# Performance work log

Measured on AMD Instinct MI355X. Metric: run time of the kernel, lower is better.

## Reference

```python
import jax, jax.numpy as jnp
import numpy as np

B, T, C, H = 2, 2048, 1024, 16
D = C // H  # head_dim = 64

def setup_inputs() -> dict:
    key = jax.random.key(0)
    k0, k1, k2, k3, k4 = jax.random.split(key, 5)
    s = 1.0 / np.sqrt(C)
    return {
        "x": jax.random.normal(k0, (B, T, C), dtype=jnp.float32),
        "w_qkv": jax.random.uniform(k1, (C, 3 * C), jnp.float32, -s, s),
        "b_qkv": jax.random.uniform(k2, (3 * C,), jnp.float32, -s, s),
        "w_proj": jax.random.uniform(k3, (C, C), jnp.float32, -s, s),
        "b_proj": jax.random.uniform(k4, (C,), jnp.float32, -s, s),
    }

def reference(x, w_qkv, b_qkv, w_proj, b_proj):
    Bx, Tx, Cx = x.shape
    qkv = x @ w_qkv + b_qkv                      # [B,T,3C]
    q, k, v = jnp.split(qkv, 3, axis=-1)
    # [B,T,C] -> [B,H,T,D]
    def heads(t):
        return t.reshape(Bx, Tx, H, D).transpose(0, 2, 1, 3)
    q, k, v = heads(q), heads(k), heads(v)
    att = jnp.einsum('bhqd,bhkd->bhqk', q, k) / np.sqrt(D).astype(np.float32)
    causal = jnp.tril(jnp.ones((Tx, Tx), dtype=bool))
    att = jnp.where(causal, att, -jnp.inf)
    att = jax.nn.softmax(att, axis=-1)
    y = jnp.einsum('bhqk,bhkd->bhqd', att, v)    # [B,H,T,D]
    y = y.transpose(0, 2, 1, 3).reshape(Bx, Tx, Cx)
    return y @ w_proj + b_proj
```

## Files before the change

kernel.cpp:

```cpp
#include <hip/hip_runtime.h>

typedef short bf16x8 __attribute__((ext_vector_type(8)));
typedef float f32x4 __attribute__((ext_vector_type(4)));
typedef unsigned short u16;
typedef unsigned short u16x8 __attribute__((ext_vector_type(8)));
typedef unsigned short u16x4 __attribute__((ext_vector_type(4), may_alias));

__device__ __forceinline__ u16 f2bf(float f) {
    union { float f; unsigned u; } v; v.f = f;
    unsigned r = v.u + 0x7fffu + ((v.u >> 16) & 1u);
    return (u16)(r >> 16);
}
__device__ __forceinline__ u16 f2bf_rhu(float f) {
    union { float f; unsigned u; } v; v.f = f;
    return (u16)((v.u + 0x8000u) >> 16);
}

__device__ __forceinline__ void gld_lds16(const void* g, void* l) {
    __builtin_amdgcn_global_load_lds(
        (const __attribute__((address_space(1))) void*)g,
        (__attribute__((address_space(3))) void*)l, 16, 0, 0);
}

__global__ __launch_bounds__(256) void x_to_bf16(const float* __restrict__ in,
                                                 u16* __restrict__ out) {
    const int i = blockIdx.x * 256 + threadIdx.x;
    float4 a = ((const float4*)in)[i * 2];
    float4 b = ((const float4*)in)[i * 2 + 1];
    u16x8 h;
    h[0] = f2bf(a.x); h[1] = f2bf(a.y); h[2] = f2bf(a.z); h[3] = f2bf(a.w);
    h[4] = f2bf(b.x); h[5] = f2bf(b.y); h[6] = f2bf(b.z); h[7] = f2bf(b.w);
    *(u16x8*)(out + (size_t)i * 8) = h;
}

__global__ __launch_bounds__(256) void transpose_w(const float* __restrict__ in,
                                                   u16* __restrict__ out,
                                                   int K, int N) {
    __shared__ float tile[32][33];
    const int n0 = blockIdx.x * 32, k0 = blockIdx.y * 32;
    const int tx = threadIdx.x, ty = threadIdx.y;
#pragma unroll
    for (int i = 0; i < 32; i += 8)
        tile[ty + i][tx] = in[(size_t)(k0 + ty + i) * N + n0 + tx];
    __syncthreads();
#pragma unroll
    for (int i = 0; i < 32; i += 8)
        out[(size_t)(n0 + ty + i) * K + k0 + tx] = f2bf(tile[tx][ty + i]);
}

#define QSCALE 0.180336880f

template <int OUTMODE, int BN>
__global__ __launch_bounds__(256) void gemm_m97(
    const u16* __restrict__ A, const u16* __restrict__ Bt,
    const float* __restrict__ bias, float* __restrict__ Cf,
    u16* __restrict__ Qo, u16* __restrict__ Ko, u16* __restrict__ Vt,
    int M, int N, int K) {
    constexpr int NF = BN / 32;
    __shared__ __align__(16) u16 lA[128 * 32];
    __shared__ __align__(16) u16 lB[BN * 32];

    const int tid = threadIdx.x;
    const int lane = tid & 63, wid = tid >> 6;
    const int wr = wid >> 1, wc = wid & 1;
    const int fr = lane & 15, fq = lane >> 4;
    const int m0 = blockIdx.y * 128, n0 = blockIdx.x * BN;

    const u16* gA = A + (size_t)(m0 + (tid >> 2)) * K + (tid & 3) * 8;
    u16* lAw = lA + wid * 512;

    const u16* gB = Bt + (size_t)(n0 + (tid >> 2)) * K + (tid & 3) * 8;
    u16* lBw = lB + wid * 512;

    f32x4 acc[4][NF];
#pragma unroll
    for (int m = 0; m < 4; m++)
#pragma unroll
        for (int n = 0; n < NF; n++)
#pragma unroll
            for (int r = 0; r < 4; r++) acc[m][n][r] = 0.f;

    for (int k0 = 0; k0 < K; k0 += 32) {
        __syncthreads();
        gld_lds16(gA + k0, lAw);
        gld_lds16(gA + (size_t)64 * K + k0, lAw + 2048);
        if (BN == 128) {
            gld_lds16(gB + k0, lBw);
            gld_lds16(gB + (size_t)64 * K + k0, lBw + 2048);
        } else {
            gld_lds16(gB + k0, lBw);
        }
        __syncthreads();

        bf16x8 a[4], b[NF];
#pragma unroll
        for (int m = 0; m < 4; m++)
            a[m] = *(const bf16x8*)&lA[(wr * 64 + m * 16 + fr) * 32 + fq * 8];
#pragma unroll
        for (int n = 0; n < NF; n++)
            b[n] = *(const bf16x8*)&lB[(wc * (BN / 2) + n * 16 + fr) * 32 + fq * 8];
#pragma unroll
        for (int m = 0; m < 4; m++)
#pragma unroll
            for (int n = 0; n < NF; n++)
                acc[m][n] = __builtin_amdgcn_mfma_f32_16x16x32_bf16(a[m], b[n], acc[m][n], 0, 0, 0);
    }

#pragma unroll
    for (int m = 0; m < 4; m++) {
#pragma unroll
        for (int n = 0; n < NF; n++) {
            const int row0 = m0 + wr * 64 + m * 16 + fq * 4;
            const int col = n0 + wc * (BN / 2) + n * 16 + fr;
            float v4[4];
#pragma unroll
            for (int r = 0; r < 4; r++) v4[r] = acc[m][n][r] + bias[col];
            if (OUTMODE == 0) {
                const int bb = row0 >> 11, t0 = row0 & 2047;
                const int sec = col >> 10, cc = col & 1023;
                const int h = cc >> 6, d = cc & 63;
                if (sec == 0) {
#pragma unroll
                    for (int r = 0; r < 4; r++)
                        Qo[(((size_t)(bb * 16 + h) * 2048 + t0 + r) << 6) + d] = f2bf(v4[r] * QSCALE);
                } else if (sec == 1) {
#pragma unroll
                    for (int r = 0; r < 4; r++)
                        Ko[(((size_t)(bb * 16 + h) * 2048 + t0 + r) << 6) + d] = f2bf(v4[r]);
                } else {
                    ushort4 p;
                    p.x = f2bf(v4[0]); p.y = f2bf(v4[1]); p.z = f2bf(v4[2]); p.w = f2bf(v4[3]);
                    *(ushort4*)&Vt[(((size_t)(bb * 16 + h) * 64 + d) << 11) + t0] = p;
                }
            } else {
#pragma unroll
                for (int r = 0; r < 4; r++)
                    Cf[(size_t)(row0 + r) * N + col] = v4[r];
            }
        }
    }
}

__global__ __launch_bounds__(256) void attn_kernel(const u16* __restrict__ Q,
                                                   const u16* __restrict__ Kg,
                                                   const u16* __restrict__ Vt,
                                                   u16* __restrict__ O) {
    __shared__ __align__(16) u16 lK[2][64 * 64];
    __shared__ __align__(16) u16 lV[2][64 * 64];
    __shared__ __align__(16) u16 lP[4][16 * 64];

    const int tid = threadIdx.x;
    const int lane = tid & 63, wid = tid >> 6;
    const int fr = lane & 15, fq = lane >> 4;
    const int bh = blockIdx.x & 31;
    const int qi = 31 - (blockIdx.x >> 5);
    const int qb0 = qi * 64;
    const size_t base = (size_t)bh * (2048 * 64);
    const u16* Qp = Q + base;
    const u16* Kp = Kg + base;
    const u16* Vp = Vt + base;

    const int q0 = qb0 + wid * 16;
    bf16x8 qa[2];
#pragma unroll
    for (int kf = 0; kf < 2; kf++)
        qa[kf] = *(const bf16x8*)&Qp[(size_t)(q0 + fr) * 64 + kf * 32 + fq * 8];
    asm volatile("s_waitcnt vmcnt(0)" ::: "memory");

    bf16x8 vones;
#pragma unroll
    for (int j = 0; j < 8; j++) vones[j] = (short)0x3F80;

    f32x4 o[4], lsum;
#pragma unroll
    for (int r = 0; r < 4; r++) {
        lsum[r] = 0.f;
#pragma unroll
        for (int n = 0; n < 4; n++) o[n][r] = 0.f;
    }

    const int srow0 = wid * 8 + (lane >> 3);
    const int gsrc = (lane & 7) ^ (lane >> 3);
    const u16* kSrc0 = Kp + (size_t)srow0 * 64 + gsrc * 8;
    const u16* vSrc0 = Vp + ((size_t)srow0 << 11) + gsrc * 8;

    const int r7 = fr & 7;
    const int gk0 = ((0 + fq) ^ r7) * 8;
    const int gk1 = ((4 + fq) ^ r7) * 8;

    const int pw_base = fr * 64 + (fq & 1) * 4;
    const int pw_gx = (fq >> 1);

    const int nt = qi + 1;

#define STAGE(buf, kt0_)                                                        \
    do {                                                                        \
        const int _kt0 = (kt0_);                                                \
        u16* _lkw = &lK[buf][wid * 512];                                        \
        u16* _lvw = &lV[buf][wid * 512];                                        \
        gld_lds16(kSrc0 + (size_t)_kt0 * 64, _lkw);                             \
        gld_lds16(kSrc0 + (size_t)(_kt0 + 32) * 64, _lkw + 2048);               \
        gld_lds16(vSrc0 + _kt0, _lvw);                                          \
        gld_lds16(vSrc0 + ((size_t)32 << 11) + _kt0, _lvw + 2048);              \
    } while (0)

    STAGE(0, 0);

    for (int kt = 0; kt < nt; kt++) {
        const int cur = kt & 1;
        if (kt + 1 < nt) {
            STAGE(cur ^ 1, (kt + 1) << 6);
            asm volatile("s_waitcnt vmcnt(4)" ::: "memory");
        } else {
            asm volatile("s_waitcnt vmcnt(0)" ::: "memory");
        }
        __builtin_amdgcn_s_barrier();

        const int kt0 = kt << 6;
        const u16* lKc = lK[cur];
        const u16* lVc = lV[cur];

        f32x4 s[4];
#pragma unroll
        for (int n = 0; n < 4; n++)
#pragma unroll
            for (int r = 0; r < 4; r++) s[n][r] = 0.f;
        __builtin_amdgcn_s_setprio(1);
#pragma unroll
        for (int n = 0; n < 4; n++) {
            bf16x8 kb0 = *(const bf16x8*)&lKc[(n * 16 + fr) * 64 + gk0];
            bf16x8 kb1 = *(const bf16x8*)&lKc[(n * 16 + fr) * 64 + gk1];
            s[n] = __builtin_amdgcn_mfma_f32_16x16x32_bf16(kb0, qa[0], s[n], 0, 0, 0);
            s[n] = __builtin_amdgcn_mfma_f32_16x16x32_bf16(kb1, qa[1], s[n], 0, 0, 0);
        }
        __builtin_amdgcn_s_setprio(0);

        if (kt == nt - 1) {
            const int qg = q0 + fr;
#pragma unroll
            for (int n = 0; n < 4; n++) {
                const int kg0 = kt0 + n * 16 + fq * 4;
#pragma unroll
                for (int r = 0; r < 4; r++)
                    if (kg0 + r > qg) s[n][r] = -200.f;
            }
        }

#pragma unroll
        for (int n = 0; n < 4; n++) {
            u16x4 w;
            w[0] = f2bf_rhu(__builtin_amdgcn_exp2f(s[n][0]));
            w[1] = f2bf_rhu(__builtin_amdgcn_exp2f(s[n][1]));
            w[2] = f2bf_rhu(__builtin_amdgcn_exp2f(s[n][2]));
            w[3] = f2bf_rhu(__builtin_amdgcn_exp2f(s[n][3]));
            const int g = ((2 * n + pw_gx) ^ r7) * 8;
            *(u16x4*)&lP[wid][pw_base + g] = w;
        }
        asm volatile("" ::: "memory");

        __builtin_amdgcn_s_setprio(1);
#pragma unroll
        for (int kf = 0; kf < 2; kf++) {
            const int gv = (kf == 0) ? gk0 : gk1;
            bf16x8 pb = *(const bf16x8*)&lP[wid][fr * 64 + gv];
            lsum = __builtin_amdgcn_mfma_f32_16x16x32_bf16(vones, pb, lsum, 0, 0, 0);
#pragma unroll
            for (int n = 0; n < 4; n++) {
                bf16x8 va = *(const bf16x8*)&lVc[(n * 16 + fr) * 64 + gv];
                o[n] = __builtin_amdgcn_mfma_f32_16x16x32_bf16(va, pb, o[n], 0, 0, 0);
            }
        }
        __builtin_amdgcn_s_setprio(0);

        __builtin_amdgcn_s_barrier();
    }
#undef STAGE

    const int bb = bh >> 4, hh = bh & 15;
    const float inv = 1.f / lsum[0];
    u16* orow = O + ((size_t)(bb * 2048 + q0 + fr)) * 1024 + hh * 64 + fq * 4;
#pragma unroll
    for (int n = 0; n < 4; n++) {
        ushort4 h;
        h.x = f2bf(o[n][0] * inv);
        h.y = f2bf(o[n][1] * inv);
        h.z = f2bf(o[n][2] * inv);
        h.w = f2bf(o[n][3] * inv);
        *(ushort4*)&orow[n * 16] = h;
    }
}

extern "C" void kernel_launch(void* const* d_in, const int* in_sizes, int n_in,
                              void* d_out, int out_size, void* d_ws, size_t ws_size,
                              hipStream_t stream) {
    const float* x      = (const float*)d_in[0];
    const float* w_qkv  = (const float*)d_in[1];
    const float* b_qkv  = (const float*)d_in[2];
    const float* w_proj = (const float*)d_in[3];
    const float* b_proj = (const float*)d_in[4];
    float* out = (float*)d_out;

    u16* ws = (u16*)d_ws;
    u16* wqkvT  = ws;
    u16* wprojT = wqkvT + 3072 * 1024;
    u16* Qb     = wprojT + 1024 * 1024;
    u16* Kb     = Qb + 32 * 2048 * 64;
    u16* Vtb    = Kb + 32 * 2048 * 64;
    u16* xb     = Vtb + 32 * 2048 * 64;
    u16* attnO  = xb;

    x_to_bf16<<<2048, 256, 0, stream>>>(x, xb);
    transpose_w<<<dim3(96, 32), dim3(32, 8), 0, stream>>>(w_qkv, wqkvT, 1024, 3072);
    transpose_w<<<dim3(32, 32), dim3(32, 8), 0, stream>>>(w_proj, wprojT, 1024, 1024);

    gemm_m97<0, 128><<<dim3(24, 32), 256, 0, stream>>>(
        xb, wqkvT, b_qkv, nullptr, Qb, Kb, Vtb, 4096, 3072, 1024);

    attn_kernel<<<1024, 256, 0, stream>>>(Qb, Kb, Vtb, attnO);

    gemm_m97<1, 64><<<dim3(16, 32), 256, 0, stream>>>(
        attnO, wprojT, b_proj, out, nullptr, nullptr, nullptr, 4096, 1024, 1024);
}
```

Baseline: 113.2 us.

## Process 128 queries per attention block, two query fragments per wave

The attention kernel now gives each block 128 query rows instead of 64, with every wave handling two 16-row query fragments. Each K tile and V fragment read from LDS is reused by both fragments, and the grid shrinks from 1024 to 512 blocks. The causal mask is now applied over the last two key tiles. The aim is to halve K/V staging and LDS read traffic per query. In exchange it uses more registers per wave and gives coarser work units, which may hurt occupancy and load balance under the causal triangle.

```diff
diff --git a/kernel.cpp b/kernel.cpp
--- a/kernel.cpp
+++ b/kernel.cpp
@@ -153,30 +153,32 @@
     const int lane = tid & 63, wid = tid >> 6;
     const int fr = lane & 15, fq = lane >> 4;
     const int bh = blockIdx.x & 31;
-    const int qi = 31 - (blockIdx.x >> 5);
-    const int qb0 = qi * 64;
+    const int qi = 15 - (blockIdx.x >> 5);
+    const int qb0 = qi * 128;
     const size_t base = (size_t)bh * (2048 * 64);
     const u16* Qp = Q + base;
     const u16* Kp = Kg + base;
     const u16* Vp = Vt + base;
 
-    const int q0 = qb0 + wid * 16;
-    bf16x8 qa[2];
-#pragma unroll
-    for (int kf = 0; kf < 2; kf++)
-        qa[kf] = *(const bf16x8*)&Qp[(size_t)(q0 + fr) * 64 + kf * 32 + fq * 8];
+    const int q0 = qb0 + wid * 32;
+    bf16x8 qa[2][2];
+#pragma unroll
+    for (int f = 0; f < 2; f++)
+#pragma unroll
+        for (int kf = 0; kf < 2; kf++)
+            qa[f][kf] = *(const bf16x8*)&Qp[(size_t)(q0 + f * 16 + fr) * 64 + kf * 32 + fq * 8];
     asm volatile("s_waitcnt vmcnt(0)" ::: "memory");
 
     bf16x8 vones;
 #pragma unroll
     for (int j = 0; j < 8; j++) vones[j] = (short)0x3F80;
 
-    f32x4 o[4], lsum;
+    f32x4 o0[4], o1[4], lsum0, lsum1;
 #pragma unroll
     for (int r = 0; r < 4; r++) {
-        lsum[r] = 0.f;
-#pragma unroll
-        for (int n = 0; n < 4; n++) o[n][r] = 0.f;
+        lsum0[r] = 0.f; lsum1[r] = 0.f;
+#pragma unroll
+        for (int n = 0; n < 4; n++) { o0[n][r] = 0.f; o1[n][r] = 0.f; }
     }
 
     const int srow0 = wid * 8 + (lane >> 3);
@@ -191,7 +193,7 @@
     const int pw_base = fr * 64 + (fq & 1) * 4;
     const int pw_gx = (fq >> 1);
 
-    const int nt = qi + 1;
+    const int nt = 2 * qi + 2;
 
 #define STAGE(buf, kt0_)                                                        \
     do {                                                                        \
@@ -204,6 +206,20 @@
         gld_lds16(vSrc0 + ((size_t)32 << 11) + _kt0, _lvw + 2048);              \
     } while (0)
 
+#define PPACK(sv)                                                               \
+    do {                                                                        \
+        _Pragma("unroll")                                                       \
+        for (int n = 0; n < 4; n++) {                                           \
+            u16x4 w;                                                            \
+            w[0] = f2bf_rhu(__builtin_amdgcn_exp2f((sv)[n][0]));                \
+            w[1] = f2bf_rhu(__builtin_amdgcn_exp2f((sv)[n][1]));                \
+            w[2] = f2bf_rhu(__builtin_amdgcn_exp2f((sv)[n][2]));                \
+            w[3] = f2bf_rhu(__builtin_amdgcn_exp2f((sv)[n][3]));                \
+            const int g = ((2 * n + pw_gx) ^ r7) * 8;                           \
+            *(u16x4*)&lP[wid][pw_base + g] = w;                                 \
+        }                                                                       \
+    } while (0)
+
     STAGE(0, 0);
 
     for (int kt = 0; kt < nt; kt++) {
@@ -220,73 +236,91 @@
         const u16* lKc = lK[cur];
         const u16* lVc = lV[cur];
 
-        f32x4 s[4];
+        f32x4 s0[4], s1[4];
 #pragma unroll
         for (int n = 0; n < 4; n++)
 #pragma unroll
-            for (int r = 0; r < 4; r++) s[n][r] = 0.f;
+            for (int r = 0; r < 4; r++) { s0[n][r] = 0.f; s1[n][r] = 0.f; }
         __builtin_amdgcn_s_setprio(1);
 #pragma unroll
         for (int n = 0; n < 4; n++) {
             bf16x8 kb0 = *(const bf16x8*)&lKc[(n * 16 + fr) * 64 + gk0];
             bf16x8 kb1 = *(const bf16x8*)&lKc[(n * 16 + fr) * 64 + gk1];
-            s[n] = __builtin_amdgcn_mfma_f32_16x16x32_bf16(kb0, qa[0], s[n], 0, 0, 0);
-            s[n] = __builtin_amdgcn_mfma_f32_16x16x32_bf16(kb1, qa[1], s[n], 0, 0, 0);
+            s0[n] = __builtin_amdgcn_mfma_f32_16x16x32_bf16(kb0, qa[0][0], s0[n], 0, 0, 0);
+            s0[n] = __builtin_amdgcn_mfma_f32_16x16x32_bf16(kb1, qa[0][1], s0[n], 0, 0, 0);
+            s1[n] = __builtin_amdgcn_mfma_f32_16x16x32_bf16(kb0, qa[1][0], s1[n], 0, 0, 0);
+            s1[n] = __builtin_amdgcn_mfma_f32_16x16x32_bf16(kb1, qa[1][1], s1[n], 0, 0, 0);
         }
         __builtin_amdgcn_s_setprio(0);
 
-        if (kt == nt - 1) {
-            const int qg = q0 + fr;
+        if (kt >= nt - 2) {
+            const int qg0 = q0 + fr, qg1 = q0 + 16 + fr;
 #pragma unroll
             for (int n = 0; n < 4; n++) {
                 const int kg0 = kt0 + n * 16 + fq * 4;
 #pragma unroll
-                for (int r = 0; r < 4; r++)
-                    if (kg0 + r > qg) s[n][r] = -200.f;
+                for (int r = 0; r < 4; r++) {
+                    if (kg0 + r > qg0) s0[n][r] = -200.f;
+                    if (kg0 + r > qg1) s1[n][r] = -200.f;
+                }
             }
         }
 
+        PPACK(s0);
+        asm volatile("" ::: "memory");
+        bf16x8 va0[4], va1[4];
 #pragma unroll
         for (int n = 0; n < 4; n++) {
-            u16x4 w;
-            w[0] = f2bf_rhu(__builtin_amdgcn_exp2f(s[n][0]));
-            w[1] = f2bf_rhu(__builtin_amdgcn_exp2f(s[n][1]));
-            w[2] = f2bf_rhu(__builtin_amdgcn_exp2f(s[n][2]));
-            w[3] = f2bf_rhu(__builtin_amdgcn_exp2f(s[n][3]));
-            const int g = ((2 * n + pw_gx) ^ r7) * 8;
-            *(u16x4*)&lP[wid][pw_base + g] = w;
-        }
+            va0[n] = *(const bf16x8*)&lVc[(n * 16 + fr) * 64 + gk0];
+            va1[n] = *(const bf16x8*)&lVc[(n * 16 + fr) * 64 + gk1];
+        }
+        bf16x8 pb00 = *(const bf16x8*)&lP[wid][fr * 64 + gk0];
+        bf16x8 pb01 = *(const bf16x8*)&lP[wid][fr * 64 + gk1];
         asm volatile("" ::: "memory");
-
         __builtin_amdgcn_s_setprio(1);
-#pragma unroll
-        for (int kf = 0; kf < 2; kf++) {
-            const int gv = (kf == 0) ? gk0 : gk1;
-            bf16x8 pb = *(const bf16x8*)&lP[wid][fr * 64 + gv];
-            lsum = __builtin_amdgcn_mfma_f32_16x16x32_bf16(vones, pb, lsum, 0, 0, 0);
-#pragma unroll
-            for (int n = 0; n < 4; n++) {
-                bf16x8 va = *(const bf16x8*)&lVc[(n * 16 + fr) * 64 + gv];
-                o[n] = __builtin_amdgcn_mfma_f32_16x16x32_bf16(va, pb, o[n], 0, 0, 0);
-            }
+        lsum0 = __builtin_amdgcn_mfma_f32_16x16x32_bf16(vones, pb00, lsum0, 0, 0, 0);
+        lsum0 = __builtin_amdgcn_mfma_f32_16x16x32_bf16(vones, pb01, lsum0, 0, 0, 0);
+#pragma unroll
+        for (int n = 0; n < 4; n++) {
+            o0[n] = __builtin_amdgcn_mfma_f32_16x16x32_bf16(va0[n], pb00, o0[n], 0, 0, 0);
+            o0[n] = __builtin_amdgcn_mfma_f32_16x16x32_bf16(va1[n], pb01, o0[n], 0, 0, 0);
         }
         __builtin_amdgcn_s_setprio(0);
 
+        PPACK(s1);
+        asm volatile("" ::: "memory");
+        bf16x8 pb10 = *(const bf16x8*)&lP[wid][fr * 64 + gk0];
+        bf16x8 pb11 = *(const bf16x8*)&lP[wid][fr * 64 + gk1];
+        asm volatile("" ::: "memory");
+        __builtin_amdgcn_s_setprio(1);
+        lsum1 = __builtin_amdgcn_mfma_f32_16x16x32_bf16(vones, pb10, lsum1, 0, 0, 0);
+        lsum1 = __builtin_amdgcn_mfma_f32_16x16x32_bf16(vones, pb11, lsum1, 0, 0, 0);
+#pragma unroll
+        for (int n = 0; n < 4; n++) {
+            o1[n] = __builtin_amdgcn_mfma_f32_16x16x32_bf16(va0[n], pb10, o1[n], 0, 0, 0);
+            o1[n] = __builtin_amdgcn_mfma_f32_16x16x32_bf16(va1[n], pb11, o1[n], 0, 0, 0);
+        }
+        __builtin_amdgcn_s_setprio(0);
+
         __builtin_amdgcn_s_barrier();
     }
 #undef STAGE
+#undef PPACK
 
     const int bb = bh >> 4, hh = bh & 15;
-    const float inv = 1.f / lsum[0];
-    u16* orow = O + ((size_t)(bb * 2048 + q0 + fr)) * 1024 + hh * 64 + fq * 4;
+    const float inv0 = 1.f / lsum0[0];
+    const float inv1 = 1.f / lsum1[0];
+    u16* orow0 = O + ((size_t)(bb * 2048 + q0 + fr)) * 1024 + hh * 64 + fq * 4;
+    u16* orow1 = O + ((size_t)(bb * 2048 + q0 + 16 + fr)) * 1024 + hh * 64 + fq * 4;
 #pragma unroll
     for (int n = 0; n < 4; n++) {
-        ushort4 h;
-        h.x = f2bf(o[n][0] * inv);
-        h.y = f2bf(o[n][1] * inv);
-        h.z = f2bf(o[n][2] * inv);
-        h.w = f2bf(o[n][3] * inv);
-        *(ushort4*)&orow[n * 16] = h;
+        ushort4 h0, h1;
+        h0.x = f2bf(o0[n][0] * inv0); h0.y = f2bf(o0[n][1] * inv0);
+        h0.z = f2bf(o0[n][2] * inv0); h0.w = f2bf(o0[n][3] * inv0);
+        *(ushort4*)&orow0[n * 16] = h0;
+        h1.x = f2bf(o1[n][0] * inv1); h1.y = f2bf(o1[n][1] * inv1);
+        h1.z = f2bf(o1[n][2] * inv1); h1.w = f2bf(o1[n][3] * inv1);
+        *(ushort4*)&orow1[n * 16] = h1;
     }
 }
 
@@ -316,7 +350,7 @@
     gemm_m97<0, 128><<<dim3(24, 32), 256, 0, stream>>>(
         xb, wqkvT, b_qkv, nullptr, Qb, Kb, Vtb, 4096, 3072, 1024);
 
-    attn_kernel<<<1024, 256, 0, stream>>>(Qb, Kb, Vtb, attnO);
+    attn_kernel<<<512, 256, 0, stream>>>(Qb, Kb, Vtb, attnO);
 
     gemm_m97<1, 64><<<dim3(16, 32), 256, 0, stream>>>(
         attnO, wprojT, b_proj, out, nullptr, nullptr, nullptr, 4096, 1024, 1024);
```

Result: slower. 125.6 us (+10.9%).
